# Performance work log

Measured on AMD Instinct MI355X. Metric: run time of the kernel, lower is better.

## Reference

```python
import jax, jax.numpy as jnp
import numpy as np

N_CAPS = 64        # num_capsules
IN_CAPS = 4096     # input_num_capsules
CAP_DIM = 32       # capsule_dimension
IN_DIM = 16        # input_capsule_dimension
NUM_ROUTINGS = 3
EPS = 1e-7         # keras.backend.epsilon()


def setup_inputs() -> dict:
    key = jax.random.key(0)
    k1, k2 = jax.random.split(key)
    input_data = jax.random.normal(k1, (IN_CAPS, IN_DIM, 1), dtype=jnp.float32)
    # RandomNormal init (stddev ~0.05 in keras v1 initializer; scale kept modest)
    W = jax.random.normal(k2, (N_CAPS, IN_CAPS, CAP_DIM, IN_DIM), dtype=jnp.float32) * 0.05
    return {"input_data": input_data, "W": W}


def reference(input_data, W):
    # u_hat = W @ input: (N, I, D, d) @ (1, I, d, 1) -> (N, I, D, 1)
    u_hat = jnp.matmul(W, input_data[None])
    u = u_hat[..., 0]  # (N, I, D)

    logits0 = jnp.zeros((N_CAPS, IN_CAPS), dtype=u.dtype)

    def body(logits, _):
        c = jax.nn.softmax(logits, axis=-1)           # over input capsules (as in source)
        s = jnp.einsum('ni,nid->nd', c, u)            # (N, D)
        # FAITHFUL: source squash uses reduce_sum over ALL axes (global norm)
        sq = jnp.sum(s * s)
        v = s * sq / (1.0 + sq) / (jnp.sqrt(sq) + EPS)  # (N, D)
        logits = logits + jnp.einsum('nid,nd->ni', u, v)
        return logits, v

    _, vs = jax.lax.scan(body, logits0, None, length=NUM_ROUTINGS)
    v = vs[-1]  # v from last iteration
    return v[..., None]  # (N, D, 1)
```

## Files before the change

kernel.cpp:

```cpp
#include <hip/hip_runtime.h>
#include <math.h>

#define N_CAPS 64
#define IN_CAPS 4096
#define CAP_DIM 32
#define IN_DIM 16
#define EPS 1e-7f

typedef float f32x4 __attribute__((ext_vector_type(4)));

static constexpr size_t U_ELEMS   = (size_t)N_CAPS * IN_CAPS * CAP_DIM;
static constexpr size_t RED_BASE  = U_ELEMS;
static constexpr size_t OFF_SACC0 = 0;
static constexpr size_t OFF_SACC1 = 2048;
static constexpr size_t OFF_SACC2 = 4096;
static constexpr size_t OFF_Z1    = 6144;
static constexpr size_t OFF_Z2    = 6208;
static constexpr size_t OFF_V     = 6272;
static constexpr int    RED_TOTAL = 6272 + 2048;

__global__ __launch_bounds__(256) void init_kernel(float* __restrict__ red) {
    for (int j = threadIdx.x; j < RED_TOTAL; j += 256) red[j] = 0.0f;
}

__global__ __launch_bounds__(256) void compute_u_kernel(
        const float* __restrict__ W, const float* __restrict__ x,
        float* __restrict__ u) {
    __shared__ __align__(16) float xs[8 * IN_DIM];
    const int tid = threadIdx.x;
    const size_t e0 = (size_t)blockIdx.x * 256;
    const int i0 = (int)((e0 >> 5) & (IN_CAPS - 1));
    if (tid < 8 * IN_DIM) xs[tid] = x[(size_t)i0 * IN_DIM + tid];
    __syncthreads();

    const int w = tid >> 6, L = tid & 63, q = L & 3, k = L >> 2;
    const size_t ebase = e0 + (size_t)w * 64;
    const f32x4* wp = (const f32x4*)W + ebase * 4;

    float res[4];
    #pragma unroll
    for (int r = 0; r < 4; ++r) {
        f32x4 wv = __builtin_nontemporal_load(wp + r * 64 + L);
        const int le = w * 64 + r * 16 + k;
        const f32x4 xv = *(const f32x4*)(xs + (le >> 5) * IN_DIM + q * 4);
        float p = wv.x * xv.x + wv.y * xv.y + wv.z * xv.z + wv.w * xv.w;
        p += __shfl_xor(p, 1, 64);
        p += __shfl_xor(p, 2, 64);
        res[r] = p;
    }
    const float outv = q == 0 ? res[0] : q == 1 ? res[1] : q == 2 ? res[2] : res[3];
    u[ebase + q * 16 + k] = outv;
}

__global__ __launch_bounds__(256) void sum_u_kernel(
        const float* __restrict__ u, float* __restrict__ s_acc) {
    __shared__ float red[256];
    const int n = blockIdx.x >> 2, chunk = blockIdx.x & 3;
    const int tid = threadIdx.x, ii = tid >> 5, d = tid & 31;
    const size_t base = ((size_t)n * IN_CAPS + (size_t)chunk * 1024) * CAP_DIM;
    float acc = 0.0f;
    for (int step = 0; step < 128; ++step)
        acc += u[base + (size_t)(step * 8 + ii) * CAP_DIM + d];
    red[tid] = acc; __syncthreads();
    for (int s = 128; s >= 32; s >>= 1) {
        if (tid < s) red[tid] += red[tid + s];
        __syncthreads();
    }
    if (tid < 32) atomicAdd(&s_acc[n * CAP_DIM + tid], red[tid]);
}

__global__ __launch_bounds__(256) void route_kernel(
        const float* __restrict__ u, const float* __restrict__ V,
        float* __restrict__ s_acc, float* __restrict__ Z) {
    __shared__ __align__(16) float vs[CAP_DIM];
    __shared__ float wbuf[256];
    __shared__ float red[256];
    const int n = blockIdx.x >> 2, chunk = blockIdx.x & 3;
    const int tid = threadIdx.x, ii = tid >> 5, d = tid & 31;
    if (tid < CAP_DIM) vs[tid] = V[n * CAP_DIM + tid];
    __syncthreads();

    const size_t ubase = (size_t)n * IN_CAPS * CAP_DIM;
    float zacc = 0.0f, sacc = 0.0f;

    for (int c = 0; c < 4; ++c) {
        const int ibase = chunk * 1024 + c * 256;
        {
            const f32x4* up = (const f32x4*)(u + ubase + (size_t)(ibase + tid) * CAP_DIM);
            const f32x4* vv = (const f32x4*)vs;
            float t = 0.0f;
            for (int q = 0; q < 8; ++q) {
                f32x4 a = up[q], b = vv[q];
                t += a.x * b.x + a.y * b.y + a.z * b.z + a.w * b.w;
            }
            float w = expf(t);
            wbuf[tid] = w;
            zacc += w;
        }
        __syncthreads();
        {
            const size_t off = ubase + (size_t)ibase * CAP_DIM;
            for (int k = 0; k < 32; ++k) {
                const int li = k * 8 + ii;
                sacc += wbuf[li] * u[off + (size_t)li * CAP_DIM + d];
            }
        }
        __syncthreads();
    }

    red[tid] = sacc; __syncthreads();
    for (int s = 128; s >= 32; s >>= 1) {
        if (tid < s) red[tid] += red[tid + s];
        __syncthreads();
    }
    if (tid < 32) atomicAdd(&s_acc[n * CAP_DIM + tid], red[tid]);
    __syncthreads();
    red[tid] = zacc; __syncthreads();
    for (int s = 128; s >= 1; s >>= 1) {
        if (tid < s) red[tid] += red[tid + s];
        __syncthreads();
    }
    if (tid == 0) atomicAdd(&Z[n], red[0]);
}

__global__ __launch_bounds__(256) void squash_kernel(
        const float* __restrict__ s_acc, const float* __restrict__ Z,
        float* __restrict__ V, float* __restrict__ out) {
    __shared__ __align__(16) float sv[N_CAPS * CAP_DIM];
    __shared__ float red[256];
    __shared__ float factor;
    const int tid = threadIdx.x;
    float psum = 0.0f;
    for (int k = 0; k < 8; ++k) {
        const int j = tid + 256 * k;
        const float scale = Z ? (1.0f / Z[j >> 5]) : (1.0f / (float)IN_CAPS);
        const float s = s_acc[j] * scale;
        sv[j] = s;
        psum += s * s;
    }
    red[tid] = psum; __syncthreads();
    for (int s = 128; s >= 1; s >>= 1) {
        if (tid < s) red[tid] += red[tid + s];
        __syncthreads();
    }
    if (tid == 0) {
        const float sq = red[0];
        factor = sq / (1.0f + sq) / (sqrtf(sq) + EPS);
    }
    __syncthreads();
    for (int k = 0; k < 8; ++k) {
        const int j = tid + 256 * k;
        const float v = sv[j] * factor;
        if (V)   V[j] += v;
        if (out) out[j] = v;
    }
}

extern "C" void kernel_launch(void* const* d_in, const int* in_sizes, int n_in,
                              void* d_out, int out_size, void* d_ws, size_t ws_size,
                              hipStream_t stream) {
    const float* x = (const float*)d_in[0];
    const float* W = (const float*)d_in[1];
    float* out = (float*)d_out;
    float* ws  = (float*)d_ws;

    float* u     = ws;
    float* redb  = ws + RED_BASE;
    float* sacc0 = redb + OFF_SACC0;
    float* sacc1 = redb + OFF_SACC1;
    float* sacc2 = redb + OFF_SACC2;
    float* Z1    = redb + OFF_Z1;
    float* Z2    = redb + OFF_Z2;
    float* V     = redb + OFF_V;

    init_kernel<<<1, 256, 0, stream>>>(redb);
    compute_u_kernel<<<(int)(U_ELEMS / 256), 256, 0, stream>>>(W, x, u);

    sum_u_kernel<<<N_CAPS * 4, 256, 0, stream>>>(u, sacc0);
    squash_kernel<<<1, 256, 0, stream>>>(sacc0, nullptr, V, nullptr);
    route_kernel<<<N_CAPS * 4, 256, 0, stream>>>(u, V, sacc1, Z1);
    squash_kernel<<<1, 256, 0, stream>>>(sacc1, Z1, V, nullptr);
    route_kernel<<<N_CAPS * 4, 256, 0, stream>>>(u, V, sacc2, Z2);
    squash_kernel<<<1, 256, 0, stream>>>(sacc2, Z2, nullptr, out);
}
```

Baseline: 720.3 us.

## Fuse routing iterations into one persistent kernel with grid barriers

Replaces the sum, route and squash kernel sequence with a single persistent routing kernel of 512 blocks that synchronises through an atomic grid barrier. Each block recomputes the global squash locally instead of relying on single-block squash kernels. Work per capsule is split into 8 chunks instead of 4, and init is replaced by a memset. This removes several launches and serial single-block steps, but depends on all 512 blocks being co-resident, since the barrier could deadlock otherwise.

```diff
diff --git a/kernel.cpp b/kernel.cpp
--- a/kernel.cpp
+++ b/kernel.cpp
@@ -16,12 +16,10 @@
 static constexpr size_t OFF_SACC2 = 4096;
 static constexpr size_t OFF_Z1    = 6144;
 static constexpr size_t OFF_Z2    = 6208;
-static constexpr size_t OFF_V     = 6272;
-static constexpr int    RED_TOTAL = 6272 + 2048;
-
-__global__ __launch_bounds__(256) void init_kernel(float* __restrict__ red) {
-    for (int j = threadIdx.x; j < RED_TOTAL; j += 256) red[j] = 0.0f;
-}
+static constexpr size_t OFF_BAR   = 6272;
+static constexpr int    RED_TOTAL = 6273;
+
+#define NBLK 512
 
 __global__ __launch_bounds__(256) void compute_u_kernel(
         const float* __restrict__ W, const float* __restrict__ x,
@@ -52,54 +50,80 @@
     u[ebase + q * 16 + k] = outv;
 }
 
-__global__ __launch_bounds__(256) void sum_u_kernel(
-        const float* __restrict__ u, float* __restrict__ s_acc) {
-    __shared__ float red[256];
-    const int n = blockIdx.x >> 2, chunk = blockIdx.x & 3;
-    const int tid = threadIdx.x, ii = tid >> 5, d = tid & 31;
-    const size_t base = ((size_t)n * IN_CAPS + (size_t)chunk * 1024) * CAP_DIM;
-    float acc = 0.0f;
-    for (int step = 0; step < 128; ++step)
-        acc += u[base + (size_t)(step * 8 + ii) * CAP_DIM + d];
-    red[tid] = acc; __syncthreads();
-    for (int s = 128; s >= 32; s >>= 1) {
-        if (tid < s) red[tid] += red[tid + s];
-        __syncthreads();
-    }
-    if (tid < 32) atomicAdd(&s_acc[n * CAP_DIM + tid], red[tid]);
-}
-
-__global__ __launch_bounds__(256) void route_kernel(
-        const float* __restrict__ u, const float* __restrict__ V,
-        float* __restrict__ s_acc, float* __restrict__ Z) {
-    __shared__ __align__(16) float vs[CAP_DIM];
-    __shared__ float wbuf[256];
-    __shared__ float red[256];
-    const int n = blockIdx.x >> 2, chunk = blockIdx.x & 3;
-    const int tid = threadIdx.x, ii = tid >> 5, d = tid & 31;
-    if (tid < CAP_DIM) vs[tid] = V[n * CAP_DIM + tid];
-    __syncthreads();
-
-    const size_t ubase = (size_t)n * IN_CAPS * CAP_DIM;
+__device__ __forceinline__ void grid_barrier(unsigned int* bar, unsigned int target) {
+    __syncthreads();
+    if (threadIdx.x == 0) {
+        __threadfence();
+        __hip_atomic_fetch_add(bar, 1u, __ATOMIC_ACQ_REL, __HIP_MEMORY_SCOPE_AGENT);
+        while (__hip_atomic_load(bar, __ATOMIC_ACQUIRE, __HIP_MEMORY_SCOPE_AGENT) < target) {
+            __builtin_amdgcn_s_sleep(2);
+        }
+    }
+    __syncthreads();
+    __threadfence();
+}
+
+__device__ __forceinline__ float aload(const float* p) {
+    return __hip_atomic_load(p, __ATOMIC_RELAXED, __HIP_MEMORY_SCOPE_AGENT);
+}
+
+__device__ __forceinline__ void squash_step(
+        const float* __restrict__ sacc, const float* __restrict__ Zp,
+        float* sred, float* zl, float* vl, int n, int tid,
+        float* __restrict__ outp) {
+    if (Zp && tid < N_CAPS) zl[tid] = aload(Zp + tid);
+    __syncthreads();
+    float psum = 0.0f;
+    #pragma unroll
+    for (int k = 0; k < 8; ++k) {
+        const int j = tid + 256 * k;
+        const float sc = Zp ? 1.0f / zl[j >> 5] : (1.0f / (float)IN_CAPS);
+        const float s = aload(sacc + j) * sc;
+        psum += s * s;
+    }
+    sred[tid] = psum; __syncthreads();
+    for (int s = 128; s >= 1; s >>= 1) {
+        if (tid < s) sred[tid] += sred[tid + s];
+        __syncthreads();
+    }
+    const float sq = sred[0];
+    const float factor = sq / (1.0f + sq) / (sqrtf(sq) + EPS);
+    __syncthreads();
+    if (tid < CAP_DIM) {
+        const float sc = Zp ? 1.0f / zl[n] : (1.0f / (float)IN_CAPS);
+        const float v = aload(sacc + n * CAP_DIM + tid) * sc * factor;
+        vl[tid] += v;
+        if (outp) outp[n * CAP_DIM + tid] = v;
+    }
+    __syncthreads();
+}
+
+__device__ __forceinline__ void route_step(
+        const float* __restrict__ u, size_t ubase, int n, int chunk, int tid,
+        const float* vl, float* wbuf, float* sred,
+        float* __restrict__ sacc_out, float* __restrict__ Zout) {
+    const int ii = tid >> 5, d = tid & 31;
     float zacc = 0.0f, sacc = 0.0f;
-
-    for (int c = 0; c < 4; ++c) {
-        const int ibase = chunk * 1024 + c * 256;
+    #pragma unroll
+    for (int c = 0; c < 2; ++c) {
+        const int ib = chunk * 512 + c * 256;
         {
-            const f32x4* up = (const f32x4*)(u + ubase + (size_t)(ibase + tid) * CAP_DIM);
-            const f32x4* vv = (const f32x4*)vs;
+            const f32x4* up = (const f32x4*)(u + ubase + (size_t)(ib + tid) * CAP_DIM);
+            const f32x4* vv = (const f32x4*)vl;
             float t = 0.0f;
+            #pragma unroll
             for (int q = 0; q < 8; ++q) {
                 f32x4 a = up[q], b = vv[q];
                 t += a.x * b.x + a.y * b.y + a.z * b.z + a.w * b.w;
             }
-            float w = expf(t);
+            const float w = expf(t);
             wbuf[tid] = w;
             zacc += w;
         }
         __syncthreads();
         {
-            const size_t off = ubase + (size_t)ibase * CAP_DIM;
+            const size_t off = ubase + (size_t)ib * CAP_DIM;
+            #pragma unroll
             for (int k = 0; k < 32; ++k) {
                 const int li = k * 8 + ii;
                 sacc += wbuf[li] * u[off + (size_t)li * CAP_DIM + d];
@@ -107,53 +131,63 @@
         }
         __syncthreads();
     }
-
-    red[tid] = sacc; __syncthreads();
+    sred[tid] = sacc; __syncthreads();
     for (int s = 128; s >= 32; s >>= 1) {
-        if (tid < s) red[tid] += red[tid + s];
-        __syncthreads();
-    }
-    if (tid < 32) atomicAdd(&s_acc[n * CAP_DIM + tid], red[tid]);
-    __syncthreads();
-    red[tid] = zacc; __syncthreads();
+        if (tid < s) sred[tid] += sred[tid + s];
+        __syncthreads();
+    }
+    if (tid < 32) atomicAdd(&sacc_out[n * CAP_DIM + tid], sred[tid]);
+    __syncthreads();
+    sred[tid] = zacc; __syncthreads();
     for (int s = 128; s >= 1; s >>= 1) {
-        if (tid < s) red[tid] += red[tid + s];
-        __syncthreads();
-    }
-    if (tid == 0) atomicAdd(&Z[n], red[0]);
-}
-
-__global__ __launch_bounds__(256) void squash_kernel(
-        const float* __restrict__ s_acc, const float* __restrict__ Z,
-        float* __restrict__ V, float* __restrict__ out) {
-    __shared__ __align__(16) float sv[N_CAPS * CAP_DIM];
-    __shared__ float red[256];
-    __shared__ float factor;
+        if (tid < s) sred[tid] += sred[tid + s];
+        __syncthreads();
+    }
+    if (tid == 0) atomicAdd(Zout + n, sred[0]);
+    __syncthreads();
+}
+
+__global__ __launch_bounds__(256) void routing_kernel(
+        const float* __restrict__ u,
+        float* __restrict__ s0, float* __restrict__ s1, float* __restrict__ s2,
+        float* __restrict__ Z1v, float* __restrict__ Z2v,
+        unsigned int* __restrict__ bar,
+        float* __restrict__ out) {
+    __shared__ __align__(16) float sred[1024];
+    __shared__ float wbuf[256];
+    __shared__ __align__(16) float vl[CAP_DIM];
+    __shared__ float zl[N_CAPS];
     const int tid = threadIdx.x;
-    float psum = 0.0f;
-    for (int k = 0; k < 8; ++k) {
-        const int j = tid + 256 * k;
-        const float scale = Z ? (1.0f / Z[j >> 5]) : (1.0f / (float)IN_CAPS);
-        const float s = s_acc[j] * scale;
-        sv[j] = s;
-        psum += s * s;
-    }
-    red[tid] = psum; __syncthreads();
-    for (int s = 128; s >= 1; s >>= 1) {
-        if (tid < s) red[tid] += red[tid + s];
-        __syncthreads();
-    }
-    if (tid == 0) {
-        const float sq = red[0];
-        factor = sq / (1.0f + sq) / (sqrtf(sq) + EPS);
-    }
-    __syncthreads();
-    for (int k = 0; k < 8; ++k) {
-        const int j = tid + 256 * k;
-        const float v = sv[j] * factor;
-        if (V)   V[j] += v;
-        if (out) out[j] = v;
-    }
+    const int bid = blockIdx.x;
+    const int n = bid >> 3, chunk = bid & 7;
+    const size_t ubase = (size_t)n * IN_CAPS * CAP_DIM;
+
+    if (tid < CAP_DIM) vl[tid] = 0.0f;
+
+    {
+        const f32x4* up = (const f32x4*)(u + ubase + (size_t)chunk * 512 * CAP_DIM);
+        f32x4 a = {0.0f, 0.0f, 0.0f, 0.0f};
+        #pragma unroll
+        for (int s = 0; s < 16; ++s) a += up[s * 256 + tid];
+        f32x4* sv = (f32x4*)sred;
+        sv[tid] = a; __syncthreads();
+        for (int off = 128; off >= 8; off >>= 1) {
+            if (tid < off) sv[tid] += sv[tid + off];
+            __syncthreads();
+        }
+        if (tid < 32) atomicAdd(&s0[n * CAP_DIM + tid], sred[tid]);
+    }
+    grid_barrier(bar, 1 * NBLK);
+
+    squash_step(s0, nullptr, sred, zl, vl, n, tid, nullptr);
+    route_step(u, ubase, n, chunk, tid, vl, wbuf, sred, s1, Z1v);
+    grid_barrier(bar, 2 * NBLK);
+
+    squash_step(s1, Z1v, sred, zl, vl, n, tid, nullptr);
+    route_step(u, ubase, n, chunk, tid, vl, wbuf, sred, s2, Z2v);
+    grid_barrier(bar, 3 * NBLK);
+
+    squash_step(s2, Z2v, sred, zl, vl, n, tid, (chunk == 0) ? out : nullptr);
 }
 
 extern "C" void kernel_launch(void* const* d_in, const int* in_sizes, int n_in,
@@ -171,15 +205,12 @@
     float* sacc2 = redb + OFF_SACC2;
     float* Z1    = redb + OFF_Z1;
     float* Z2    = redb + OFF_Z2;
-    float* V     = redb + OFF_V;
-
-    init_kernel<<<1, 256, 0, stream>>>(redb);
+    unsigned int* bar = (unsigned int*)(redb + OFF_BAR);
+
+    hipMemsetAsync(redb, 0, RED_TOTAL * sizeof(float), stream);
+
     compute_u_kernel<<<(int)(U_ELEMS / 256), 256, 0, stream>>>(W, x, u);
 
-    sum_u_kernel<<<N_CAPS * 4, 256, 0, stream>>>(u, sacc0);
-    squash_kernel<<<1, 256, 0, stream>>>(sacc0, nullptr, V, nullptr);
-    route_kernel<<<N_CAPS * 4, 256, 0, stream>>>(u, V, sacc1, Z1);
-    squash_kernel<<<1, 256, 0, stream>>>(sacc1, Z1, V, nullptr);
-    route_kernel<<<N_CAPS * 4, 256, 0, stream>>>(u, V, sacc2, Z2);
-    squash_kernel<<<1, 256, 0, stream>>>(sacc2, Z2, nullptr, out);
-}
+    routing_kernel<<<NBLK, 256, 0, stream>>>(u, sacc0, sacc1, sacc2,
+                                             Z1, Z2, bar, out);
+}
```

Result: slower. 904.5 us (+25.6%).
